# Kernel tuning notes

Measured on AMD Instinct MI355X. Metric: run time of the kernel, lower is better.

The kernel has to match this reference:

```python
import jax, jax.numpy as jnp
import numpy as np

N_SRC, N_DST, E, D, H = 100000, 10000, 320000, 128, 128
LN_EPS = 1e-5


def setup_inputs() -> dict:
    key = jax.random.key(0)
    ks = jax.random.split(key, 12)
    h_src = jax.random.normal(ks[0], (N_SRC, D), jnp.float32)
    h_dst = jax.random.normal(ks[1], (N_DST, D), jnp.float32)
    s_emb = jax.random.normal(ks[2], (N_DST, D), jnp.float32)
    edge_weight = jax.random.uniform(ks[3], (E,), jnp.float32)
    src_idx = jax.random.randint(ks[4], (E,), 0, N_SRC)
    dst_idx = jnp.sort(jax.random.randint(ks[5], (E,), 0, N_DST))
    # session_attention: Linear(2D->H, no bias) -> tanh -> Linear(H->1, no bias)
    W1 = jax.random.normal(ks[6], (2 * D, H), jnp.float32) / np.sqrt(2 * D)
    w2 = jax.random.normal(ks[7], (H,), jnp.float32) / np.sqrt(H)
    # output_proj: Linear(2D->D) with bias
    Wo = jax.random.normal(ks[8], (2 * D, D), jnp.float32) / np.sqrt(2 * D)
    bo = jnp.zeros((D,), jnp.float32)
    gamma = jnp.ones((D,), jnp.float32)
    beta = jnp.zeros((D,), jnp.float32)
    return {"h_src": h_src, "h_dst": h_dst, "s_emb": s_emb,
            "edge_weight": edge_weight, "src_idx": src_idx, "dst_idx": dst_idx,
            "W1": W1, "w2": w2, "Wo": Wo, "bo": bo, "gamma": gamma, "beta": beta}


def reference(h_src, h_dst, s_emb, edge_weight, src_idx, dst_idx, W1, w2, Wo, bo, gamma, beta):
    d = h_src.shape[1]
    # concat([h_src[src], s_emb[dst]]) @ W1 == h_src[src] @ W1[:d] + s_emb[dst] @ W1[d:]
    # project per-node first (cheaper than per-edge concat matmul)
    p_src = h_src @ W1[:d]          # [N_src, H]
    p_dst = s_emb @ W1[d:]          # [N_dst, H]
    raw = jnp.tanh(p_src[src_idx] + p_dst[dst_idx]) @ w2   # [E]
    raw = raw * edge_weight
    # edge_softmax: segment softmax over incoming edges of each dst node
    seg_max = jax.ops.segment_max(raw, dst_idx, num_segments=h_dst.shape[0])
    seg_max = jnp.where(jnp.isfinite(seg_max), seg_max, 0.0)  # handle degree-0 dsts
    ex = jnp.exp(raw - seg_max[dst_idx])
    den = jax.ops.segment_sum(ex, dst_idx, num_segments=h_dst.shape[0])
    attn = ex / den[dst_idx]                                 # [E]
    # u_mul_e + sum: weighted gather-scatter aggregation
    h_global = jax.ops.segment_sum(h_src[src_idx] * attn[:, None], dst_idx,
                                   num_segments=h_dst.shape[0])  # [N_dst, D]
    # output_proj on concat([h_dst, h_global])
    out = h_dst @ Wo[:d] + h_global @ Wo[d:] + bo
    # residual + layer norm (dropout = identity in eval)
    x = h_dst + out
    mu = jnp.mean(x, axis=-1, keepdims=True)
    var = jnp.mean((x - mu) ** 2, axis=-1, keepdims=True)
    y = (x - mu) / jnp.sqrt(var + LN_EPS) * gamma + beta
    return (y, attn[:, None])
```

## Files before the change

### kernel.cpp

```cpp
#include <hip/hip_runtime.h>
#include <math.h>

#define D128 128
#define SCAPW 256

typedef unsigned int uint32;
typedef unsigned short ushort_t;
typedef short bf16x8 __attribute__((ext_vector_type(8)));
typedef float f32x4 __attribute__((ext_vector_type(4)));
typedef float f32x2 __attribute__((ext_vector_type(2)));

__device__ __forceinline__ ushort_t bf16_of(float x) {
  uint32 u = __float_as_uint(x);
  return (ushort_t)((u + 0x7fffu + ((u >> 16) & 1u)) >> 16);
}
__device__ __forceinline__ uint32 pack_bf2(float x, float y) {
  uint32 bx = __float_as_uint(x);
  uint32 by = __float_as_uint(y);
  bx = (bx + 0x7fffu + ((bx >> 16) & 1u)) >> 16;
  by = (by + 0x7fffu + ((by >> 16) & 1u)) & 0xffff0000u;
  return bx | by;
}

__device__ __forceinline__ float fast_tanh(float x) {
  float e = __expf(2.0f * x);
  float r = __builtin_amdgcn_rcpf(1.0f + e);
  return fmaf(-2.0f, r, 1.0f);
}

__device__ __forceinline__ uint32 pack_fp8x4(float a, float b, float c, float d) {
  int u = __builtin_amdgcn_cvt_pk_fp8_f32(a, b, 0, false);
  u = __builtin_amdgcn_cvt_pk_fp8_f32(c, d, u, true);
  return (uint32)u;
}

__device__ __forceinline__ bf16x8 bf16x8_of(float4 a, float4 c) {
  union { uint4 u; bf16x8 h; } r;
  r.u.x = pack_bf2(a.x, a.y);
  r.u.y = pack_bf2(a.z, a.w);
  r.u.z = pack_bf2(c.x, c.y);
  r.u.w = pack_bf2(c.z, c.w);
  return r.h;
}

__global__ __launch_bounds__(256) void prep_all(
    const float* __restrict__ W1, const float* __restrict__ Wo,
    const int* __restrict__ dst_idx,
    ushort_t* __restrict__ Wfrag, ushort_t* __restrict__ Wo_frag,
    int* __restrict__ off, int E, int N) {
  const int b = blockIdx.x;
  const int tid = threadIdx.x;
  if (b < 16) {
    int t = b * 256 + tid;
    int lane = t & 63;
    int kc = (t >> 6) & 3;
    int nt = (t >> 8) & 7;
    int h = (t >> 11) & 1;
    int m = lane & 15;
    int quad = lane >> 4;
    int krow = h * D128 + kc * 32 + quad * 8;
    int ncol = nt * 16 + m;
    ushort_t fr[8];
#pragma unroll
    for (int j = 0; j < 8; j++) fr[j] = bf16_of(W1[(size_t)(krow + j) * D128 + ncol]);
    *(uint4*)(Wfrag + (size_t)t * 8) = *(const uint4*)fr;
  } else if (b < 32) {
    int t = (b - 16) * 256 + tid;
    int lane = t & 63;
    int kc = (t >> 6) & 7;
    int nt = (t >> 9) & 7;
    int m = lane & 15;
    int quad = lane >> 4;
    int krow = kc * 32 + quad * 8;
    int ncol = nt * 16 + m;
    ushort_t fr[8];
#pragma unroll
    for (int j = 0; j < 8; j++) fr[j] = bf16_of(Wo[(size_t)(krow + j) * D128 + ncol]);
    *(uint4*)(Wo_frag + (size_t)t * 8) = *(const uint4*)fr;
  } else {
    int e = (b - 32) * 256 + tid;
    if (e >= E) return;
    int d = dst_idx[e];
    int dprev = (e == 0) ? -1 : dst_idx[e - 1];
    for (int v = dprev + 1; v <= d; v++) off[v] = e;
    if (e == E - 1) {
      for (int v = d + 1; v <= N; v++) off[v] = E;
    }
  }
}

__global__ __launch_bounds__(256) void gemm_mfma(
    const float* __restrict__ Xa, const float* __restrict__ Xb,
    const ushort_t* __restrict__ Wfrag,
    uint32* __restrict__ Pa, uint32* __restrict__ Pb,
    uint32* __restrict__ x_f8,
    int Ma, int Mb, int nblk_a) {
  __shared__ uint32 Ys8[64][36];
  const int blk = blockIdx.x;
  const float* X;
  const bf16x8* Wf;
  uint32* P;
  int M, row0;
  bool emit8;
  if (blk < nblk_a) {
    X = Xa; P = Pa; Wf = (const bf16x8*)Wfrag;           M = Ma; row0 = blk * 64; emit8 = true;
  } else {
    X = Xb; P = Pb; Wf = (const bf16x8*)(Wfrag + 16384); M = Mb; row0 = (blk - nblk_a) * 64; emit8 = false;
  }

  const int tid = threadIdx.x;
  const int wave = tid >> 6;
  const int lane = tid & 63;
  const int m = lane & 15;
  const int quad = lane >> 4;

  const int ra = min(row0 + wave * 16 + m, M - 1);
  const float* xp = X + (size_t)ra * D128 + quad * 8;

  float4 xf[8];
#pragma unroll
  for (int kc = 0; kc < 4; kc++) {
    xf[kc * 2]     = *(const float4*)(xp + kc * 32);
    xf[kc * 2 + 1] = *(const float4*)(xp + kc * 32 + 4);
  }

  f32x4 acc[8];
#pragma unroll
  for (int nt = 0; nt < 8; nt++) acc[nt] = (f32x4){0.f, 0.f, 0.f, 0.f};

#pragma unroll
  for (int kc = 0; kc < 4; kc++) {
    bf16x8 x0 = bf16x8_of(xf[kc * 2], xf[kc * 2 + 1]);
    if (emit8) {
      uint2 q;
      q.x = pack_fp8x4(xf[kc * 2].x, xf[kc * 2].y, xf[kc * 2].z, xf[kc * 2].w);
      q.y = pack_fp8x4(xf[kc * 2 + 1].x, xf[kc * 2 + 1].y, xf[kc * 2 + 1].z, xf[kc * 2 + 1].w);
      *(uint2*)(x_f8 + (size_t)ra * 32 + kc * 8 + quad * 2) = q;
    }
#pragma unroll
    for (int nt = 0; nt < 8; nt++) {
      bf16x8 wf = Wf[(nt * 4 + kc) * 64 + lane];
      acc[nt] = __builtin_amdgcn_mfma_f32_16x16x32_bf16(wf, x0, acc[nt], 0, 0, 0);
    }
  }

#pragma unroll
  for (int nt = 0; nt < 8; nt++)
    Ys8[wave * 16 + m][nt * 4 + quad] =
        pack_fp8x4(acc[nt][0], acc[nt][1], acc[nt][2], acc[nt][3]);
  __syncthreads();

#pragma unroll
  for (int it = 0; it < 2; it++) {
    int f = tid + 256 * it;
    int row = f >> 3;
    int cu = (f & 7) * 4;
    int grow = row0 + row;
    if (grow < M) *(uint4*)(P + (size_t)grow * 32 + cu) = *(const uint4*)(&Ys8[row][cu]);
  }
}

__global__ __launch_bounds__(256) void attn_agg_kernel(
    const uint32* __restrict__ p_src_f8, const uint32* __restrict__ p_dst_f8,
    const float* __restrict__ w2, const float* __restrict__ ew,
    const int* __restrict__ src_idx, const int* __restrict__ off,
    const uint32* __restrict__ h_src_f8,
    float* __restrict__ attn_out, uint32* __restrict__ h_glob_bf, int N_dst) {
  const int tid = threadIdx.x;
  const int wv = tid >> 6;
  const int lane = tid & 63;
  const int v = blockIdx.x * 4 + wv;

  __shared__ float sex[4][SCAPW];
  __shared__ int ssrc[4][SCAPW];
  if (v >= N_dst) return;

  const int lo = off[v], hi = off[v + 1];
  const int deg = hi - lo;
  const int sub = lane & 15;
  const int eg = lane >> 4;
  const bool fast = (deg <= SCAPW);

  float4 wA = *(const float4*)(w2 + sub * 8);
  float4 wB = *(const float4*)(w2 + sub * 8 + 4);
  uint2 pdu = *(const uint2*)(p_dst_f8 + (size_t)v * 32 + sub * 2);
  f32x2 pd0 = __builtin_amdgcn_cvt_pk_f32_fp8(pdu.x, false);
  f32x2 pd1 = __builtin_amdgcn_cvt_pk_f32_fp8(pdu.x, true);
  f32x2 pd2 = __builtin_amdgcn_cvt_pk_f32_fp8(pdu.y, false);
  f32x2 pd3 = __builtin_amdgcn_cvt_pk_f32_fp8(pdu.y, true);

  float den = 0.f;
  for (int base = 0; base < deg; base += 4) {
    const int ei = base + eg;
    float ex = 0.f;
    if (ei < deg) {
      const int e = lo + ei;
      const int s = src_idx[e];
      const float ewv = ew[e];
      uint2 us = *(const uint2*)(p_src_f8 + (size_t)s * 32 + sub * 2);
      f32x2 a0 = __builtin_amdgcn_cvt_pk_f32_fp8(us.x, false);
      f32x2 a1 = __builtin_amdgcn_cvt_pk_f32_fp8(us.x, true);
      f32x2 a2 = __builtin_amdgcn_cvt_pk_f32_fp8(us.y, false);
      f32x2 a3 = __builtin_amdgcn_cvt_pk_f32_fp8(us.y, true);
      float sc;
      sc = fast_tanh(a0.x + pd0.x) * wA.x;
      sc = fmaf(fast_tanh(a0.y + pd0.y), wA.y, sc);
      sc = fmaf(fast_tanh(a1.x + pd1.x), wA.z, sc);
      sc = fmaf(fast_tanh(a1.y + pd1.y), wA.w, sc);
      sc = fmaf(fast_tanh(a2.x + pd2.x), wB.x, sc);
      sc = fmaf(fast_tanh(a2.y + pd2.y), wB.y, sc);
      sc = fmaf(fast_tanh(a3.x + pd3.x), wB.z, sc);
      sc = fmaf(fast_tanh(a3.y + pd3.y), wB.w, sc);
#pragma unroll
      for (int o = 1; o <= 8; o <<= 1) sc += __shfl_xor(sc, o, 64);
      ex = __expf(sc * ewv);
      if (sub == 0) {
        if (fast) { sex[wv][ei] = ex; ssrc[wv][ei] = s; }
        else attn_out[lo + ei] = ex;
      }
    }
    den += (sub == 0) ? ex : 0.f;
  }
#pragma unroll
  for (int o = 1; o <= 32; o <<= 1) den += __shfl_xor(den, o, 64);
  const float inv = (deg > 0) ? 1.0f / den : 0.0f;

  const int c4 = lane & 31;
  const int hw = lane >> 5;
  float a0 = 0.f, a1 = 0.f, a2 = 0.f, a3 = 0.f;

  if (fast) {
    const int pad = (deg + 15) & ~15;
    for (int i = deg + lane; i < pad; i += 64) { sex[wv][i] = 0.f; ssrc[wv][i] = 0; }
    for (int i = lane; i < deg; i += 64) attn_out[lo + i] = sex[wv][i] * inv;
    for (int b = 0; b < pad; b += 16) {
#pragma unroll
      for (int j = 0; j < 8; j++) {
        const int idx = b + j * 2 + hw;
        float ex = sex[wv][idx];
        int s = ssrc[wv][idx];
        uint32 u = h_src_f8[(size_t)s * 32 + c4];
        f32x2 h0 = __builtin_amdgcn_cvt_pk_f32_fp8(u, false);
        f32x2 h1 = __builtin_amdgcn_cvt_pk_f32_fp8(u, true);
        a0 = fmaf(ex, h0.x, a0);
        a1 = fmaf(ex, h0.y, a1);
        a2 = fmaf(ex, h1.x, a2);
        a3 = fmaf(ex, h1.y, a3);
      }
    }
  } else {
    for (int b = 0; b < deg; b += 16) {
#pragma unroll
      for (int j = 0; j < 8; j++) {
        const int idx = b + j * 2 + hw;
        float ex = 0.f;
        int s = 0;
        if (idx < deg) { ex = attn_out[lo + idx]; s = src_idx[lo + idx]; }
        uint32 u = h_src_f8[(size_t)s * 32 + c4];
        f32x2 h0 = __builtin_amdgcn_cvt_pk_f32_fp8(u, false);
        f32x2 h1 = __builtin_amdgcn_cvt_pk_f32_fp8(u, true);
        a0 = fmaf(ex, h0.x, a0);
        a1 = fmaf(ex, h0.y, a1);
        a2 = fmaf(ex, h1.x, a2);
        a3 = fmaf(ex, h1.y, a3);
      }
    }
    for (int i = lane; i < deg; i += 64) attn_out[lo + i] *= inv;
  }

  a0 += __shfl_xor(a0, 32, 64);
  a1 += __shfl_xor(a1, 32, 64);
  a2 += __shfl_xor(a2, 32, 64);
  a3 += __shfl_xor(a3, 32, 64);
  if (hw == 0) {
    uint2 o;
    o.x = pack_bf2(a0 * inv, a1 * inv);
    o.y = pack_bf2(a2 * inv, a3 * inv);
    *(uint2*)(h_glob_bf + (size_t)v * 64 + c4 * 2) = o;
  }
}

__global__ __launch_bounds__(128) void out_mfma_ln(
    const float* __restrict__ h_dst, const ushort_t* __restrict__ h_glob_bf,
    const ushort_t* __restrict__ Wo_frag,
    const float* __restrict__ bo,
    const float* __restrict__ gamma, const float* __restrict__ beta,
    float* __restrict__ y, int N) {
  __shared__ float sbo[128], sgam[128], sbet[128];
  const int tid = threadIdx.x;
  if (tid < 128) { sbo[tid] = bo[tid]; sgam[tid] = gamma[tid]; sbet[tid] = beta[tid]; }
  __syncthreads();

  const int w = tid >> 6;
  const int lane = tid & 63;
  const int m = lane & 15;
  const int quad = lane >> 4;
  const int row0 = blockIdx.x * 32 + w * 16;
  const int ra = min(row0 + m, N - 1);
  const bf16x8* Wf = (const bf16x8*)Wo_frag;

  f32x4 acc[8];
#pragma unroll
  for (int nt = 0; nt < 8; nt++) acc[nt] = (f32x4){0.f, 0.f, 0.f, 0.f};

#pragma unroll
  for (int kc = 0; kc < 8; kc++) {
    bf16x8 a;
    if (kc < 4) {
      const float* p = h_dst + (size_t)ra * D128 + kc * 32 + quad * 8;
      float4 f0 = *(const float4*)p;
      float4 f1 = *(const float4*)(p + 4);
      a = bf16x8_of(f0, f1);
    } else {
      a = *(const bf16x8*)(h_glob_bf + (size_t)ra * D128 + (kc & 3) * 32 + quad * 8);
    }
#pragma unroll
    for (int nt = 0; nt < 8; nt++) {
      bf16x8 bfr = Wf[(nt * 8 + kc) * 64 + lane];
      acc[nt] = __builtin_amdgcn_mfma_f32_16x16x32_bf16(a, bfr, acc[nt], 0, 0, 0);
    }
  }

#pragma unroll
  for (int r = 0; r < 4; r++) {
    const int grow = row0 + quad * 4 + r;
    const int gr = min(grow, N - 1);
    float x[8];
    float s1 = 0.f, s2 = 0.f;
#pragma unroll
    for (int nt = 0; nt < 8; nt++) {
      float hd = h_dst[(size_t)gr * D128 + nt * 16 + m];
      float xv = hd + acc[nt][r] + sbo[nt * 16 + m];
      x[nt] = xv;
      s1 += xv;
      s2 = fmaf(xv, xv, s2);
    }
#pragma unroll
    for (int o = 1; o <= 8; o <<= 1) {
      s1 += __shfl_xor(s1, o, 64);
      s2 += __shfl_xor(s2, o, 64);
    }
    float mu = s1 * (1.0f / 128.0f);
    float var = s2 * (1.0f / 128.0f) - mu * mu;
    float rstd = __builtin_amdgcn_rcpf(sqrtf(var + 1e-5f));
    if (grow < N) {
#pragma unroll
      for (int nt = 0; nt < 8; nt++) {
        int c = nt * 16 + m;
        y[(size_t)grow * D128 + c] = (x[nt] - mu) * rstd * sgam[c] + sbet[c];
      }
    }
  }
}

extern "C" void kernel_launch(void* const* d_in, const int* in_sizes, int n_in,
                              void* d_out, int out_size, void* d_ws, size_t ws_size,
                              hipStream_t stream) {
  const float* h_src = (const float*)d_in[0];
  const float* h_dst = (const float*)d_in[1];
  const float* s_emb = (const float*)d_in[2];
  const float* ew    = (const float*)d_in[3];
  const int* src_idx = (const int*)d_in[4];
  const int* dst_idx = (const int*)d_in[5];
  const float* W1    = (const float*)d_in[6];
  const float* w2    = (const float*)d_in[7];
  const float* Wo    = (const float*)d_in[8];
  const float* bo    = (const float*)d_in[9];
  const float* gamma = (const float*)d_in[10];
  const float* beta  = (const float*)d_in[11];

  const int N_src = in_sizes[0] / D128;
  const int N_dst = in_sizes[1] / D128;
  const int E = in_sizes[3];

  float* out_y = (float*)d_out;
  float* out_attn = out_y + (size_t)N_dst * D128;

  uint32* p_src_f8 = (uint32*)d_ws;
  uint32* p_dst_f8 = p_src_f8 + (size_t)N_src * 32;
  uint32* h_src_f8 = p_dst_f8 + (size_t)N_dst * 32;
  uint32* h_glob_bf = h_src_f8 + (size_t)N_src * 32;
  int* seg_off = (int*)(h_glob_bf + (size_t)N_dst * 64);
  ushort_t* Wfrag = (ushort_t*)(seg_off + N_dst + 1 + 3);
  ushort_t* Wo_frag = Wfrag + 32768;

  const int nblk_a = (N_src + 63) / 64;
  const int nblk_b = (N_dst + 63) / 64;
  const int nb_seg = (E + 255) / 256;

  prep_all<<<32 + nb_seg, 256, 0, stream>>>(
      W1, Wo, dst_idx, Wfrag, Wo_frag, seg_off, E, N_dst);
  gemm_mfma<<<nblk_a + nblk_b, 256, 0, stream>>>(
      h_src, s_emb, Wfrag, p_src_f8, p_dst_f8, h_src_f8, N_src, N_dst, nblk_a);
  attn_agg_kernel<<<(N_dst + 3) / 4, 256, 0, stream>>>(
      p_src_f8, p_dst_f8, w2, ew, src_idx, seg_off, h_src_f8, out_attn,
      h_glob_bf, N_dst);
  out_mfma_ln<<<(N_dst + 31) / 32, 128, 0, stream>>>(
      h_dst, (const ushort_t*)h_glob_bf, Wo_frag,
      bo, gamma, beta, out_y, N_dst);
}
```

Before: 165.4 us.

## Stage GEMM weights in LDS, unroll edge scoring by two, prefetch output-proj inputs

The projection GEMM now copies the 32KB weight fragment block into shared memory once per block, instead of each wave reading it from global memory inside the MFMA loop. The LDS buffer is then reused for the fp8 output staging. The attention kernel processes two edges per lane group per iteration, issuing both gathers before computing, which adds memory-level parallelism. The output-projection kernel loads all h_dst and h_glob fragments up front, before the MFMA loop. These changes raise LDS and register use, which may lower occupancy.

```diff
diff --git a/kernel.cpp b/kernel.cpp
--- a/kernel.cpp
+++ b/kernel.cpp
@@ -41,6 +41,24 @@
   r.u.z = pack_bf2(c.x, c.y);
   r.u.w = pack_bf2(c.z, c.w);
   return r.h;
+}
+
+__device__ __forceinline__ float score8(uint2 us, f32x2 pd0, f32x2 pd1, f32x2 pd2,
+                                        f32x2 pd3, float4 wA, float4 wB) {
+  f32x2 a0 = __builtin_amdgcn_cvt_pk_f32_fp8(us.x, false);
+  f32x2 a1 = __builtin_amdgcn_cvt_pk_f32_fp8(us.x, true);
+  f32x2 a2 = __builtin_amdgcn_cvt_pk_f32_fp8(us.y, false);
+  f32x2 a3 = __builtin_amdgcn_cvt_pk_f32_fp8(us.y, true);
+  float sc;
+  sc = fast_tanh(a0.x + pd0.x) * wA.x;
+  sc = fmaf(fast_tanh(a0.y + pd0.y), wA.y, sc);
+  sc = fmaf(fast_tanh(a1.x + pd1.x), wA.z, sc);
+  sc = fmaf(fast_tanh(a1.y + pd1.y), wA.w, sc);
+  sc = fmaf(fast_tanh(a2.x + pd2.x), wB.x, sc);
+  sc = fmaf(fast_tanh(a2.y + pd2.y), wB.y, sc);
+  sc = fmaf(fast_tanh(a3.x + pd3.x), wB.z, sc);
+  sc = fmaf(fast_tanh(a3.y + pd3.y), wB.w, sc);
+  return sc;
 }
 
 __global__ __launch_bounds__(256) void prep_all(
@@ -95,17 +113,17 @@
     uint32* __restrict__ Pa, uint32* __restrict__ Pb,
     uint32* __restrict__ x_f8,
     int Ma, int Mb, int nblk_a) {
-  __shared__ uint32 Ys8[64][36];
+  __shared__ uint4 WL[2048];
   const int blk = blockIdx.x;
   const float* X;
-  const bf16x8* Wf;
+  const uint4* Wg;
   uint32* P;
   int M, row0;
   bool emit8;
   if (blk < nblk_a) {
-    X = Xa; P = Pa; Wf = (const bf16x8*)Wfrag;           M = Ma; row0 = blk * 64; emit8 = true;
+    X = Xa; P = Pa; Wg = (const uint4*)Wfrag;             M = Ma; row0 = blk * 64; emit8 = true;
   } else {
-    X = Xb; P = Pb; Wf = (const bf16x8*)(Wfrag + 16384); M = Mb; row0 = (blk - nblk_a) * 64; emit8 = false;
+    X = Xb; P = Pb; Wg = (const uint4*)(Wfrag + 16384);   M = Mb; row0 = (blk - nblk_a) * 64; emit8 = false;
   }
 
   const int tid = threadIdx.x;
@@ -124,29 +142,45 @@
     xf[kc * 2 + 1] = *(const float4*)(xp + kc * 32 + 4);
   }
 
-  f32x4 acc[8];
-#pragma unroll
-  for (int nt = 0; nt < 8; nt++) acc[nt] = (f32x4){0.f, 0.f, 0.f, 0.f};
-
-#pragma unroll
-  for (int kc = 0; kc < 4; kc++) {
-    bf16x8 x0 = bf16x8_of(xf[kc * 2], xf[kc * 2 + 1]);
-    if (emit8) {
+  uint4 wtmp[8];
+#pragma unroll
+  for (int j = 0; j < 8; j++) wtmp[j] = Wg[tid + 256 * j];
+#pragma unroll
+  for (int j = 0; j < 8; j++) WL[tid + 256 * j] = wtmp[j];
+
+  if (emit8) {
+#pragma unroll
+    for (int kc = 0; kc < 4; kc++) {
       uint2 q;
       q.x = pack_fp8x4(xf[kc * 2].x, xf[kc * 2].y, xf[kc * 2].z, xf[kc * 2].w);
       q.y = pack_fp8x4(xf[kc * 2 + 1].x, xf[kc * 2 + 1].y, xf[kc * 2 + 1].z, xf[kc * 2 + 1].w);
       *(uint2*)(x_f8 + (size_t)ra * 32 + kc * 8 + quad * 2) = q;
     }
+  }
+  bf16x8 xb[4];
+#pragma unroll
+  for (int kc = 0; kc < 4; kc++) xb[kc] = bf16x8_of(xf[kc * 2], xf[kc * 2 + 1]);
+
+  __syncthreads();
+
+  f32x4 acc[8];
+#pragma unroll
+  for (int nt = 0; nt < 8; nt++) acc[nt] = (f32x4){0.f, 0.f, 0.f, 0.f};
+
+#pragma unroll
+  for (int kc = 0; kc < 4; kc++) {
 #pragma unroll
     for (int nt = 0; nt < 8; nt++) {
-      bf16x8 wf = Wf[(nt * 4 + kc) * 64 + lane];
-      acc[nt] = __builtin_amdgcn_mfma_f32_16x16x32_bf16(wf, x0, acc[nt], 0, 0, 0);
-    }
-  }
-
+      bf16x8 wf = *(const bf16x8*)&WL[(nt * 4 + kc) * 64 + lane];
+      acc[nt] = __builtin_amdgcn_mfma_f32_16x16x32_bf16(wf, xb[kc], acc[nt], 0, 0, 0);
+    }
+  }
+
+  __syncthreads();
+  uint32* Ys = (uint32*)WL;
 #pragma unroll
   for (int nt = 0; nt < 8; nt++)
-    Ys8[wave * 16 + m][nt * 4 + quad] =
+    Ys[(wave * 16 + m) * 36 + nt * 4 + quad] =
         pack_fp8x4(acc[nt][0], acc[nt][1], acc[nt][2], acc[nt][3]);
   __syncthreads();
 
@@ -156,7 +190,7 @@
     int row = f >> 3;
     int cu = (f & 7) * 4;
     int grow = row0 + row;
-    if (grow < M) *(uint4*)(P + (size_t)grow * 32 + cu) = *(const uint4*)(&Ys8[row][cu]);
+    if (grow < M) *(uint4*)(P + (size_t)grow * 32 + cu) = *(const uint4*)(&Ys[row * 36 + cu]);
   }
 }
 
@@ -190,36 +224,49 @@
   f32x2 pd3 = __builtin_amdgcn_cvt_pk_f32_fp8(pdu.y, true);
 
   float den = 0.f;
-  for (int base = 0; base < deg; base += 4) {
-    const int ei = base + eg;
-    float ex = 0.f;
-    if (ei < deg) {
-      const int e = lo + ei;
-      const int s = src_idx[e];
-      const float ewv = ew[e];
-      uint2 us = *(const uint2*)(p_src_f8 + (size_t)s * 32 + sub * 2);
-      f32x2 a0 = __builtin_amdgcn_cvt_pk_f32_fp8(us.x, false);
-      f32x2 a1 = __builtin_amdgcn_cvt_pk_f32_fp8(us.x, true);
-      f32x2 a2 = __builtin_amdgcn_cvt_pk_f32_fp8(us.y, false);
-      f32x2 a3 = __builtin_amdgcn_cvt_pk_f32_fp8(us.y, true);
-      float sc;
-      sc = fast_tanh(a0.x + pd0.x) * wA.x;
-      sc = fmaf(fast_tanh(a0.y + pd0.y), wA.y, sc);
-      sc = fmaf(fast_tanh(a1.x + pd1.x), wA.z, sc);
-      sc = fmaf(fast_tanh(a1.y + pd1.y), wA.w, sc);
-      sc = fmaf(fast_tanh(a2.x + pd2.x), wB.x, sc);
-      sc = fmaf(fast_tanh(a2.y + pd2.y), wB.y, sc);
-      sc = fmaf(fast_tanh(a3.x + pd3.x), wB.z, sc);
-      sc = fmaf(fast_tanh(a3.y + pd3.y), wB.w, sc);
+  for (int base = 0; base < deg; base += 8) {
+    const int ei0 = base + eg;
+    const int ei1 = base + 4 + eg;
+    const bool v0 = ei0 < deg;
+    const bool v1 = ei1 < deg;
+    int s0 = 0, s1 = 0;
+    float ew0 = 0.f, ew1 = 0.f;
+    uint2 us0, us1;
+    us0.x = us0.y = us1.x = us1.y = 0u;
+    if (v0) {
+      const int e = lo + ei0;
+      s0 = src_idx[e];
+      ew0 = ew[e];
+      us0 = *(const uint2*)(p_src_f8 + (size_t)s0 * 32 + sub * 2);
+    }
+    if (v1) {
+      const int e = lo + ei1;
+      s1 = src_idx[e];
+      ew1 = ew[e];
+      us1 = *(const uint2*)(p_src_f8 + (size_t)s1 * 32 + sub * 2);
+    }
+    float ex0 = 0.f, ex1 = 0.f;
+    if (v0) {
+      float sc = score8(us0, pd0, pd1, pd2, pd3, wA, wB);
 #pragma unroll
       for (int o = 1; o <= 8; o <<= 1) sc += __shfl_xor(sc, o, 64);
-      ex = __expf(sc * ewv);
+      ex0 = __expf(sc * ew0);
       if (sub == 0) {
-        if (fast) { sex[wv][ei] = ex; ssrc[wv][ei] = s; }
-        else attn_out[lo + ei] = ex;
+        if (fast) { sex[wv][ei0] = ex0; ssrc[wv][ei0] = s0; }
+        else attn_out[lo + ei0] = ex0;
       }
     }
-    den += (sub == 0) ? ex : 0.f;
+    if (v1) {
+      float sc = score8(us1, pd0, pd1, pd2, pd3, wA, wB);
+#pragma unroll
+      for (int o = 1; o <= 8; o <<= 1) sc += __shfl_xor(sc, o, 64);
+      ex1 = __expf(sc * ew1);
+      if (sub == 0) {
+        if (fast) { sex[wv][ei1] = ex1; ssrc[wv][ei1] = s1; }
+        else attn_out[lo + ei1] = ex1;
+      }
+    }
+    den += (sub == 0) ? (ex0 + ex1) : 0.f;
   }
 #pragma unroll
   for (int o = 1; o <= 32; o <<= 1) den += __shfl_xor(den, o, 64);
@@ -299,21 +346,25 @@
   const int ra = min(row0 + m, N - 1);
   const bf16x8* Wf = (const bf16x8*)Wo_frag;
 
+  float4 f0[4], f1[4];
+  bf16x8 ag[4];
+#pragma unroll
+  for (int kc = 0; kc < 4; kc++) {
+    const float* p = h_dst + (size_t)ra * D128 + kc * 32 + quad * 8;
+    f0[kc] = *(const float4*)p;
+    f1[kc] = *(const float4*)(p + 4);
+  }
+#pragma unroll
+  for (int kc = 0; kc < 4; kc++)
+    ag[kc] = *(const bf16x8*)(h_glob_bf + (size_t)ra * D128 + kc * 32 + quad * 8);
+
   f32x4 acc[8];
 #pragma unroll
   for (int nt = 0; nt < 8; nt++) acc[nt] = (f32x4){0.f, 0.f, 0.f, 0.f};
 
 #pragma unroll
   for (int kc = 0; kc < 8; kc++) {
-    bf16x8 a;
-    if (kc < 4) {
-      const float* p = h_dst + (size_t)ra * D128 + kc * 32 + quad * 8;
-      float4 f0 = *(const float4*)p;
-      float4 f1 = *(const float4*)(p + 4);
-      a = bf16x8_of(f0, f1);
-    } else {
-      a = *(const bf16x8*)(h_glob_bf + (size_t)ra * D128 + (kc & 3) * 32 + quad * 8);
-    }
+    bf16x8 a = (kc < 4) ? bf16x8_of(f0[kc & 3], f1[kc & 3]) : ag[kc & 3];
 #pragma unroll
     for (int nt = 0; nt < 8; nt++) {
       bf16x8 bfr = Wf[(nt * 8 + kc) * 64 + lane];
```

New measurement: 163.0 us. No clear change (-1.5%).
